# Kernel tuning notes

Measured on AMD Instinct MI355X. Metric: run time of the kernel, lower is better.

The kernel has to match this reference:

```python
import jax, jax.numpy as jnp
import numpy as np

B, S, HID, NH, DH = 2, 2048, 1024, 16, 64
NEG = jnp.float32(-1e-09)  # faithful to source: tiny negative, NOT -1e9


def _linear_params(key, fan_in, fan_out):
    k1, k2 = jax.random.split(key)
    lim = 1.0 / np.sqrt(fan_in)
    W = jax.random.uniform(k1, (fan_out, fan_in), jnp.float32, -lim, lim)
    b = jax.random.uniform(k2, (fan_out,), jnp.float32, -lim, lim)
    return W, b


def setup_inputs() -> dict:
    key = jax.random.key(0)
    ks = jax.random.split(key, 7)
    Q = jax.random.normal(ks[0], (B, S, HID), jnp.float32)
    K = jax.random.normal(ks[1], (B, S, HID), jnp.float32)
    V = jax.random.normal(ks[2], (B, S, HID), jnp.float32)
    pad_mask = jnp.ones((B, S), jnp.float32)
    attn_mask = jnp.tril(jnp.ones((S, S), jnp.float32))  # causal
    Wq, bq = _linear_params(ks[3], HID, HID)
    Wk, bk = _linear_params(ks[4], HID, HID)
    Wv, bv = _linear_params(ks[5], HID, HID)
    Wo, bo = _linear_params(ks[6], HID, HID)
    return {"Q": Q, "K": K, "V": V, "pad_mask": pad_mask, "attn_mask": attn_mask,
            "Wq": Wq, "bq": bq, "Wk": Wk, "bk": bk, "Wv": Wv, "bv": bv,
            "Wo": Wo, "bo": bo}


def reference(Q, K, V, pad_mask, attn_mask, Wq, bq, Wk, bk, Wv, bv, Wo, bo):
    def split_heads(x):  # [B,S,HID] -> [B,NH,S,DH]; matches torch.split+stack
        return x.reshape(B, S, NH, DH).transpose(0, 2, 1, 3)

    q = split_heads(Q @ Wq.T + bq)
    k = split_heads(K @ Wk.T + bk)
    v = split_heads(V @ Wv.T + bv)

    scores = jnp.einsum('bhqd,bhkd->bhqk', q, k) / np.sqrt(DH)
    # combined mask: pad outer-product * attn_mask (broadcast [S,S] -> [B,S,S])
    mask = pad_mask[:, :, None] * pad_mask[:, None, :] * attn_mask
    scores = jnp.where(mask[:, None, :, :] != 0, scores, NEG)
    attn = jax.nn.softmax(scores, axis=-1)

    ctx = jnp.einsum('bhqk,bhkd->bhqd', attn, v)
    ctx = ctx.transpose(0, 2, 1, 3).reshape(B, S, HID)  # concat heads
    return ctx @ Wo.T + bo
```

## Files before the change

### kernel.cpp

```cpp
#include <hip/hip_runtime.h>
#include <math.h>

#define BATCH 2
#define SLEN  2048
#define HIDD  1024
#define NHEAD 16
#define DHEAD 64
#define NEGV  (-1e-09f)

typedef __attribute__((ext_vector_type(8))) short bf16x8;
typedef __attribute__((ext_vector_type(4))) float f32x4;
typedef unsigned short u16;
typedef unsigned long long u64;

__device__ __forceinline__ u16 f2bf(float x) {
    unsigned u = __builtin_bit_cast(unsigned, x);
    return (u16)((u + 0x7fffu + ((u >> 16) & 1u)) >> 16);
}

#define GLD16(gp, lp) __builtin_amdgcn_global_load_lds(                      \
    (__attribute__((address_space(1))) void*)(gp),                           \
    (__attribute__((address_space(3))) void*)(lp), 16, 0, 0)

__global__ __launch_bounds__(256) void cvt_kernel(
    const float* __restrict__ s0, const float* __restrict__ s1,
    const float* __restrict__ s2, const float* __restrict__ s3,
    const float* __restrict__ s4, const float* __restrict__ s5,
    const float* __restrict__ s6,
    u16* __restrict__ d0, u16* __restrict__ d1, u16* __restrict__ d2,
    u16* __restrict__ d3, u16* __restrict__ d4, u16* __restrict__ d5,
    u16* __restrict__ d6)
{
    const float* sp; u16* dp; int n;
    switch (blockIdx.z) {
        case 0: sp = s0; dp = d0; n = 4194304; break;
        case 1: sp = s1; dp = d1; n = 4194304; break;
        case 2: sp = s2; dp = d2; n = 4194304; break;
        case 3: sp = s3; dp = d3; n = 1048576; break;
        case 4: sp = s4; dp = d4; n = 1048576; break;
        case 5: sp = s5; dp = d5; n = 1048576; break;
        default: sp = s6; dp = d6; n = 1048576; break;
    }
    const int idx = (blockIdx.x * 256 + threadIdx.x) * 8;
    if (idx >= n) return;
    const float4 a = *(const float4*)(sp + idx);
    const float4 c = *(const float4*)(sp + idx + 4);
    union { bf16x8 v; u16 u[8]; } o;
    o.u[0] = f2bf(a.x); o.u[1] = f2bf(a.y); o.u[2] = f2bf(a.z); o.u[3] = f2bf(a.w);
    o.u[4] = f2bf(c.x); o.u[5] = f2bf(c.y); o.u[6] = f2bf(c.z); o.u[7] = f2bf(c.w);
    *(bf16x8*)(dp + idx) = o.v;
}

template<int MODE>
__device__ __forceinline__ void gemm128(const u16* __restrict__ A,
                                        const u16* __restrict__ W,
                                        const float* __restrict__ bias,
                                        void* __restrict__ outp)
{
    __shared__ __align__(16) u16 sA[4096];
    __shared__ __align__(16) u16 sB[4096];
    const int t  = threadIdx.x;
    const int l  = t & 63, w = t >> 6;
    const int wr = w >> 1, wc = w & 1;
    const int m0 = blockIdx.y * 128, n0 = blockIdx.x * 128;

    f32x4 acc[4][4];
#pragma unroll
    for (int i = 0; i < 4; ++i)
#pragma unroll
        for (int j = 0; j < 4; ++j) acc[i][j] = (f32x4){0.f, 0.f, 0.f, 0.f};

    const int srow = t >> 2;
    const int scol = (t & 3) * 8;
    const u16* Ap = A + (size_t)(m0 + srow) * HIDD + scol;
    const u16* Wp = W + (size_t)(n0 + srow) * HIDD + scol;

    for (int k0 = 0; k0 < HIDD; k0 += 32) {
        __syncthreads();
        GLD16(Ap + k0,                      &sA[t * 8]);
        GLD16(Ap + k0 + (size_t)64 * HIDD,  &sA[2048 + t * 8]);
        GLD16(Wp + k0,                      &sB[t * 8]);
        GLD16(Wp + k0 + (size_t)64 * HIDD,  &sB[2048 + t * 8]);
        __syncthreads();

        bf16x8 af[4], bg[4];
#pragma unroll
        for (int i = 0; i < 4; ++i) {
            af[i] = *(const bf16x8*)&sA[(wr * 64 + i * 16 + (l & 15)) * 32 + (l >> 4) * 8];
            bg[i] = *(const bf16x8*)&sB[(wc * 64 + i * 16 + (l & 15)) * 32 + (l >> 4) * 8];
        }
#pragma unroll
        for (int mi = 0; mi < 4; ++mi)
#pragma unroll
            for (int ni = 0; ni < 4; ++ni)
                acc[mi][ni] = __builtin_amdgcn_mfma_f32_16x16x32_bf16(
                                  af[mi], bg[ni], acc[mi][ni], 0, 0, 0);
    }

    float bb[4];
#pragma unroll
    for (int ni = 0; ni < 4; ++ni) bb[ni] = bias[n0 + wc * 64 + ni * 16 + (l & 15)];

#pragma unroll
    for (int mi = 0; mi < 4; ++mi) {
#pragma unroll
        for (int ni = 0; ni < 4; ++ni) {
            const int n = n0 + wc * 64 + ni * 16 + (l & 15);
#pragma unroll
            for (int r = 0; r < 4; ++r) {
                const int m = m0 + wr * 64 + mi * 16 + (l >> 4) * 4 + r;
                const float v = acc[mi][ni][r] + bb[ni];
                if (MODE == 0) {
                    const int b = m >> 11, s = m & (SLEN - 1);
                    const int h = n >> 6,  d = n & (DHEAD - 1);
                    ((u16*)outp)[(((size_t)(b * NHEAD + h)) * SLEN + s) * DHEAD + d] = f2bf(v);
                } else {
                    ((float*)outp)[(size_t)m * HIDD + n] = v;
                }
            }
        }
    }
}

__global__ __launch_bounds__(256) void qkv_kernel(
    const u16* __restrict__ Qb, const u16* __restrict__ Kb, const u16* __restrict__ Vb,
    const u16* __restrict__ Wqb, const u16* __restrict__ Wkb, const u16* __restrict__ Wvb,
    const float* __restrict__ bq, const float* __restrict__ bk, const float* __restrict__ bv,
    u16* __restrict__ qh, u16* __restrict__ kh, u16* __restrict__ vh)
{
    if (blockIdx.z == 0)      gemm128<0>(Qb, Wqb, bq, qh);
    else if (blockIdx.z == 1) gemm128<0>(Kb, Wkb, bk, kh);
    else                      gemm128<0>(Vb, Wvb, bv, vh);
}

__global__ __launch_bounds__(256) void outproj_kernel(
    const u16* __restrict__ Cb, const u16* __restrict__ Wob,
    const float* __restrict__ bo, float* __restrict__ out)
{
    gemm128<1>(Cb, Wob, bo, out);
}

__global__ __launch_bounds__(256) void vtrans_kernel(const u16* __restrict__ vh,
                                                     u16* __restrict__ vt)
{
    const int bh = blockIdx.y, st = blockIdx.x, t = threadIdx.x;
    const u16* src = vh + ((size_t)bh * SLEN + st * 64) * DHEAD;
    u16* dst = vt + (size_t)bh * DHEAD * SLEN + st * 64;
    __shared__ u16 Ts[64][72];
#pragma unroll
    for (int it = 0; it < 2; ++it) {
        const int slot = t + it * 256;
        const int s = slot >> 3, c = (slot & 7) * 8;
        union { bf16x8 v; u16 u[8]; } x;
        x.v = *(const bf16x8*)(src + s * DHEAD + c);
#pragma unroll
        for (int j = 0; j < 8; ++j) Ts[c + j][s] = x.u[j];
    }
    __syncthreads();
#pragma unroll
    for (int it = 0; it < 2; ++it) {
        const int slot = t + it * 256;
        const int d = slot >> 3, c = (slot & 7) * 8;
        union { bf16x8 v; u16 u[8]; } x;
#pragma unroll
        for (int j = 0; j < 8; ++j) x.u[j] = Ts[d][c + j];
        *(bf16x8*)(dst + (size_t)d * SLEN + c) = x.v;
    }
}

__global__ __launch_bounds__(256) void mask_kernel(const float* __restrict__ pad,
                                                   const float* __restrict__ am,
                                                   u64* __restrict__ mb)
{
    const int gid = blockIdx.x * 256 + threadIdx.x;
    const int c = gid & 31;
    const int s = (gid >> 5) & (SLEN - 1);
    const int b = gid >> 16;
    const float padq = pad[b * SLEN + s];
    const float* amrow = am + (size_t)s * SLEN + c * 64;
    const float* pkp   = pad + b * SLEN + c * 64;
    u64 bits = 0;
#pragma unroll
    for (int j0 = 0; j0 < 64; j0 += 4) {
        const float4 a  = *(const float4*)(amrow + j0);
        const float4 pk = *(const float4*)(pkp + j0);
        if (padq * pk.x * a.x != 0.f) bits |= (1ull << (j0 + 0));
        if (padq * pk.y * a.y != 0.f) bits |= (1ull << (j0 + 1));
        if (padq * pk.z * a.z != 0.f) bits |= (1ull << (j0 + 2));
        if (padq * pk.w * a.w != 0.f) bits |= (1ull << (j0 + 3));
    }
    mb[((size_t)b * SLEN + s) * 32 + c] = bits;
}

__global__ __launch_bounds__(256) void flash_kernel(
    const u16* __restrict__ qh, const u16* __restrict__ kh,
    const u16* __restrict__ vt, const u64* __restrict__ mb,
    u16* __restrict__ cb)
{
    __shared__ __align__(16) char smem[24576];
    const int qt = blockIdx.x, h = blockIdx.y, b = blockIdx.z;
    const int t = threadIdx.x, l = t & 63, w = t >> 6;
    const int head = b * NHEAD + h;
    const u16* qp = qh + ((size_t)head * SLEN + qt * 64) * DHEAD;
    const u16* kp = kh + (size_t)head * SLEN * DHEAD;
    const u16* vp = vt + (size_t)head * DHEAD * SLEN;

    bf16x8 qf[2];
#pragma unroll
    for (int ks = 0; ks < 2; ++ks)
        qf[ks] = *(const bf16x8*)(qp + (w * 16 + (l & 15)) * DHEAD
                                     + ks * 32 + (l >> 4) * 8);

    f32x4 oacc[4];
    float mrun[4], lrun[4];
#pragma unroll
    for (int i = 0; i < 4; ++i) {
        oacc[i] = (f32x4){0.f, 0.f, 0.f, 0.f};
        mrun[i] = -INFINITY; lrun[i] = 0.f;
    }

    const int scb = (t & 7) * 16;

    for (int kt = 0; kt < SLEN / 64; ++kt) {
        bf16x8 kv[2], vv[2];
#pragma unroll
        for (int it = 0; it < 2; ++it) {
            const int row = (t >> 3) + it * 32;
            kv[it] = *(const bf16x8*)(kp + ((size_t)(kt * 64 + row)) * DHEAD + scb / 2);
            vv[it] = *(const bf16x8*)(vp + (size_t)row * SLEN + kt * 64 + scb / 2);
        }
        __syncthreads();
#pragma unroll
        for (int it = 0; it < 2; ++it) {
            const int row  = (t >> 3) + it * 32;
            const int byte = row * 128 + (scb ^ ((row & 7) << 4));
            *(bf16x8*)(smem + byte)        = kv[it];
            *(bf16x8*)(smem + 8192 + byte) = vv[it];
        }
        __syncthreads();

        f32x4 s4[4];
#pragma unroll
        for (int nf = 0; nf < 4; ++nf) s4[nf] = (f32x4){0.f, 0.f, 0.f, 0.f};
#pragma unroll
        for (int ks = 0; ks < 2; ++ks) {
#pragma unroll
            for (int nf = 0; nf < 4; ++nf) {
                const int kr = nf * 16 + (l & 15);
                const bf16x8 kf = *(const bf16x8*)(smem + kr * 128 +
                        ((ks * 64 + (l >> 4) * 16) ^ ((kr & 7) << 4)));
                s4[nf] = __builtin_amdgcn_mfma_f32_16x16x32_bf16(qf[ks], kf, s4[nf], 0, 0, 0);
            }
        }

        const int rbase = qt * 64 + w * 16 + (l >> 4) * 4;
        u64 bits[4];
#pragma unroll
        for (int r = 0; r < 4; ++r)
            bits[r] = mb[((size_t)b * SLEN + rbase + r) * 32 + kt];
#pragma unroll
        for (int r = 0; r < 4; ++r) {
            float sv[4];
#pragma unroll
            for (int nf = 0; nf < 4; ++nf) {
                const int bit = nf * 16 + (l & 15);
                sv[nf] = ((bits[r] >> bit) & 1ull) ? s4[nf][r] * 0.125f : NEGV;
            }
            float rm = fmaxf(fmaxf(sv[0], sv[1]), fmaxf(sv[2], sv[3]));
            rm = fmaxf(rm, __shfl_xor(rm, 1));
            rm = fmaxf(rm, __shfl_xor(rm, 2));
            rm = fmaxf(rm, __shfl_xor(rm, 4));
            rm = fmaxf(rm, __shfl_xor(rm, 8));
            const float mnew = fmaxf(mrun[r], rm);
            const float corr = __expf(mrun[r] - mnew);
            float p[4], rs = 0.f;
#pragma unroll
            for (int nf = 0; nf < 4; ++nf) { p[nf] = __expf(sv[nf] - mnew); rs += p[nf]; }
            rs += __shfl_xor(rs, 1);
            rs += __shfl_xor(rs, 2);
            rs += __shfl_xor(rs, 4);
            rs += __shfl_xor(rs, 8);
            lrun[r] = lrun[r] * corr + rs;
            mrun[r] = mnew;
#pragma unroll
            for (int nf = 0; nf < 4; ++nf) oacc[nf][r] *= corr;
            const int prow = (l >> 4) * 4 + r;
#pragma unroll
            for (int nf = 0; nf < 4; ++nf) {
                const int col = nf * 16 + (l & 15);
                *(u16*)(smem + 16384 + w * 2048 + prow * 128 +
                        ((col * 2) ^ ((prow & 7) << 4))) = f2bf(p[nf]);
            }
        }

#pragma unroll
        for (int ks = 0; ks < 2; ++ks) {
            const bf16x8 pf = *(const bf16x8*)(smem + 16384 + w * 2048 + (l & 15) * 128 +
                    ((ks * 64 + (l >> 4) * 16) ^ ((l & 7) << 4)));
#pragma unroll
            for (int nf = 0; nf < 4; ++nf) {
                const int vr = nf * 16 + (l & 15);
                const bf16x8 vf = *(const bf16x8*)(smem + 8192 + vr * 128 +
                        ((ks * 64 + (l >> 4) * 16) ^ ((vr & 7) << 4)));
                oacc[nf] = __builtin_amdgcn_mfma_f32_16x16x32_bf16(pf, vf, oacc[nf], 0, 0, 0);
            }
        }
        __syncthreads();
    }

#pragma unroll
    for (int r = 0; r < 4; ++r) {
        const float inv = 1.f / lrun[r];
        const int srow = qt * 64 + w * 16 + (l >> 4) * 4 + r;
#pragma unroll
        for (int nf = 0; nf < 4; ++nf) {
            const float v = oacc[nf][r] * inv;
            cb[((size_t)b * SLEN + srow) * HIDD + h * DHEAD + nf * 16 + (l & 15)] = f2bf(v);
        }
    }
}

extern "C" void kernel_launch(void* const* d_in, const int* in_sizes, int n_in,
                              void* d_out, int out_size, void* d_ws, size_t ws_size,
                              hipStream_t stream)
{
    (void)in_sizes; (void)n_in; (void)out_size; (void)ws_size;
    const float* Q   = (const float*)d_in[0];
    const float* K   = (const float*)d_in[1];
    const float* V   = (const float*)d_in[2];
    const float* pad = (const float*)d_in[3];
    const float* am  = (const float*)d_in[4];
    const float* Wq  = (const float*)d_in[5];
    const float* bq  = (const float*)d_in[6];
    const float* Wk  = (const float*)d_in[7];
    const float* bk  = (const float*)d_in[8];
    const float* Wv  = (const float*)d_in[9];
    const float* bv  = (const float*)d_in[10];
    const float* Wo  = (const float*)d_in[11];
    const float* bo  = (const float*)d_in[12];
    float* out = (float*)d_out;

    char* ws = (char*)d_ws;
    const size_t MB = 1u << 20;
    u16* Qb  = (u16*)(ws + 0);
    u16* Kb  = (u16*)(ws + 8  * MB);
    u16* Vb  = (u16*)(ws + 16 * MB);
    u16* Wqb = (u16*)(ws + 24 * MB);
    u16* Wkb = (u16*)(ws + 26 * MB);
    u16* Wvb = (u16*)(ws + 28 * MB);
    u16* Wob = (u16*)(ws + 30 * MB);
    u16* qhp = (u16*)(ws + 32 * MB);
    u16* khp = (u16*)(ws + 40 * MB);
    u16* vhp = (u16*)(ws + 48 * MB);
    u16* vtp = (u16*)(ws + 56 * MB);
    u64* mbp = (u64*)(ws + 64 * MB);
    u16* cbp = (u16*)(ws + 0);

    cvt_kernel<<<dim3(2048, 1, 7), 256, 0, stream>>>(Q, K, V, Wq, Wk, Wv, Wo,
                                                     Qb, Kb, Vb, Wqb, Wkb, Wvb, Wob);
    qkv_kernel<<<dim3(8, 32, 3), 256, 0, stream>>>(Qb, Kb, Vb, Wqb, Wkb, Wvb,
                                                   bq, bk, bv, qhp, khp, vhp);
    vtrans_kernel<<<dim3(32, 32), 256, 0, stream>>>(vhp, vtp);
    mask_kernel<<<dim3(512), 256, 0, stream>>>(pad, am, mbp);
    flash_kernel<<<dim3(32, 16, 2), 256, 0, stream>>>(qhp, khp, vtp, mbp, cbp);
    outproj_kernel<<<dim3(8, 32, 1), 256, 0, stream>>>(cbp, Wob, bo, out);
}
```

Measured before the change: 328.6 us.

## Compute transposed scores so each lane owns one query row for softmax

The QK^T MFMA now takes its operands in swapped order, producing S^T, so each lane holds all scores for a single query row. The online-softmax max and sum then need only two cross-lane shuffles per tile instead of four per row for four rows, and the mask needs one 64-bit load per lane instead of four. Per-row correction and normalisation factors are broadcast back to the output layout with __shfl. The trailing per-iteration __syncthreads is removed, relying on the barrier before the next shared-memory write to protect K/V reuse.

```diff
diff --git a/kernel.cpp b/kernel.cpp
--- a/kernel.cpp
+++ b/kernel.cpp
@@ -200,24 +200,22 @@
     __shared__ __align__(16) char smem[24576];
     const int qt = blockIdx.x, h = blockIdx.y, b = blockIdx.z;
     const int t = threadIdx.x, l = t & 63, w = t >> 6;
+    const int q = l & 15, hi = l >> 4;
     const int head = b * NHEAD + h;
     const u16* qp = qh + ((size_t)head * SLEN + qt * 64) * DHEAD;
     const u16* kp = kh + (size_t)head * SLEN * DHEAD;
     const u16* vp = vt + (size_t)head * DHEAD * SLEN;
+    const u64* mrow = mb + ((size_t)b * SLEN + qt * 64 + w * 16 + q) * 32;
 
     bf16x8 qf[2];
 #pragma unroll
     for (int ks = 0; ks < 2; ++ks)
-        qf[ks] = *(const bf16x8*)(qp + (w * 16 + (l & 15)) * DHEAD
-                                     + ks * 32 + (l >> 4) * 8);
+        qf[ks] = *(const bf16x8*)(qp + (w * 16 + q) * DHEAD + ks * 32 + hi * 8);
 
     f32x4 oacc[4];
-    float mrun[4], lrun[4];
-#pragma unroll
-    for (int i = 0; i < 4; ++i) {
-        oacc[i] = (f32x4){0.f, 0.f, 0.f, 0.f};
-        mrun[i] = -INFINITY; lrun[i] = 0.f;
-    }
+#pragma unroll
+    for (int i = 0; i < 4; ++i) oacc[i] = (f32x4){0.f, 0.f, 0.f, 0.f};
+    float mq = -INFINITY, lq = 0.f;
 
     const int scb = (t & 7) * 16;
 
@@ -239,83 +237,87 @@
         }
         __syncthreads();
 
-        f32x4 s4[4];
-#pragma unroll
-        for (int nf = 0; nf < 4; ++nf) s4[nf] = (f32x4){0.f, 0.f, 0.f, 0.f};
+        f32x4 s4t[4];
+#pragma unroll
+        for (int nf = 0; nf < 4; ++nf) s4t[nf] = (f32x4){0.f, 0.f, 0.f, 0.f};
 #pragma unroll
         for (int ks = 0; ks < 2; ++ks) {
 #pragma unroll
             for (int nf = 0; nf < 4; ++nf) {
-                const int kr = nf * 16 + (l & 15);
+                const int kr = nf * 16 + q;
                 const bf16x8 kf = *(const bf16x8*)(smem + kr * 128 +
-                        ((ks * 64 + (l >> 4) * 16) ^ ((kr & 7) << 4)));
-                s4[nf] = __builtin_amdgcn_mfma_f32_16x16x32_bf16(qf[ks], kf, s4[nf], 0, 0, 0);
-            }
-        }
-
-        const int rbase = qt * 64 + w * 16 + (l >> 4) * 4;
-        u64 bits[4];
-#pragma unroll
-        for (int r = 0; r < 4; ++r)
-            bits[r] = mb[((size_t)b * SLEN + rbase + r) * 32 + kt];
+                        ((ks * 64 + hi * 16) ^ ((kr & 7) << 4)));
+                s4t[nf] = __builtin_amdgcn_mfma_f32_16x16x32_bf16(kf, qf[ks], s4t[nf], 0, 0, 0);
+            }
+        }
+
+        const u64 bits = mrow[kt];
+        float p[4][4];
+        float rm = -INFINITY;
+#pragma unroll
+        for (int nf = 0; nf < 4; ++nf)
+#pragma unroll
+            for (int r = 0; r < 4; ++r) {
+                const int bit = nf * 16 + hi * 4 + r;
+                const float svv = ((bits >> bit) & 1ull) ? s4t[nf][r] * 0.125f : NEGV;
+                p[nf][r] = svv;
+                rm = fmaxf(rm, svv);
+            }
+        rm = fmaxf(rm, __shfl_xor(rm, 16));
+        rm = fmaxf(rm, __shfl_xor(rm, 32));
+        const float mnew = fmaxf(mq, rm);
+        const float corrq = __expf(mq - mnew);
+        float rs = 0.f;
+#pragma unroll
+        for (int nf = 0; nf < 4; ++nf)
+#pragma unroll
+            for (int r = 0; r < 4; ++r) {
+                p[nf][r] = __expf(p[nf][r] - mnew);
+                rs += p[nf][r];
+            }
+        rs += __shfl_xor(rs, 16);
+        rs += __shfl_xor(rs, 32);
+        lq = lq * corrq + rs;
+        mq = mnew;
+
+#pragma unroll
+        for (int nf = 0; nf < 4; ++nf)
+#pragma unroll
+            for (int r = 0; r < 4; ++r) {
+                const int kpos = nf * 16 + hi * 4 + r;
+                *(u16*)(smem + 16384 + w * 2048 + q * 128 +
+                        ((kpos * 2) ^ ((q & 7) << 4))) = f2bf(p[nf][r]);
+            }
+
 #pragma unroll
         for (int r = 0; r < 4; ++r) {
-            float sv[4];
+            const float cr = __shfl(corrq, hi * 4 + r);
+#pragma unroll
+            for (int nf = 0; nf < 4; ++nf) oacc[nf][r] *= cr;
+        }
+
+#pragma unroll
+        for (int ks = 0; ks < 2; ++ks) {
+            const bf16x8 pf = *(const bf16x8*)(smem + 16384 + w * 2048 + q * 128 +
+                    ((ks * 64 + hi * 16) ^ ((q & 7) << 4)));
 #pragma unroll
             for (int nf = 0; nf < 4; ++nf) {
-                const int bit = nf * 16 + (l & 15);
-                sv[nf] = ((bits[r] >> bit) & 1ull) ? s4[nf][r] * 0.125f : NEGV;
-            }
-            float rm = fmaxf(fmaxf(sv[0], sv[1]), fmaxf(sv[2], sv[3]));
-            rm = fmaxf(rm, __shfl_xor(rm, 1));
-            rm = fmaxf(rm, __shfl_xor(rm, 2));
-            rm = fmaxf(rm, __shfl_xor(rm, 4));
-            rm = fmaxf(rm, __shfl_xor(rm, 8));
-            const float mnew = fmaxf(mrun[r], rm);
-            const float corr = __expf(mrun[r] - mnew);
-            float p[4], rs = 0.f;
-#pragma unroll
-            for (int nf = 0; nf < 4; ++nf) { p[nf] = __expf(sv[nf] - mnew); rs += p[nf]; }
-            rs += __shfl_xor(rs, 1);
-            rs += __shfl_xor(rs, 2);
-            rs += __shfl_xor(rs, 4);
-            rs += __shfl_xor(rs, 8);
-            lrun[r] = lrun[r] * corr + rs;
-            mrun[r] = mnew;
-#pragma unroll
-            for (int nf = 0; nf < 4; ++nf) oacc[nf][r] *= corr;
-            const int prow = (l >> 4) * 4 + r;
-#pragma unroll
-            for (int nf = 0; nf < 4; ++nf) {
-                const int col = nf * 16 + (l & 15);
-                *(u16*)(smem + 16384 + w * 2048 + prow * 128 +
-                        ((col * 2) ^ ((prow & 7) << 4))) = f2bf(p[nf]);
-            }
-        }
-
-#pragma unroll
-        for (int ks = 0; ks < 2; ++ks) {
-            const bf16x8 pf = *(const bf16x8*)(smem + 16384 + w * 2048 + (l & 15) * 128 +
-                    ((ks * 64 + (l >> 4) * 16) ^ ((l & 7) << 4)));
-#pragma unroll
-            for (int nf = 0; nf < 4; ++nf) {
-                const int vr = nf * 16 + (l & 15);
+                const int vr = nf * 16 + q;
                 const bf16x8 vf = *(const bf16x8*)(smem + 8192 + vr * 128 +
-                        ((ks * 64 + (l >> 4) * 16) ^ ((vr & 7) << 4)));
+                        ((ks * 64 + hi * 16) ^ ((vr & 7) << 4)));
                 oacc[nf] = __builtin_amdgcn_mfma_f32_16x16x32_bf16(pf, vf, oacc[nf], 0, 0, 0);
             }
         }
-        __syncthreads();
     }
 
 #pragma unroll
     for (int r = 0; r < 4; ++r) {
-        const float inv = 1.f / lrun[r];
-        const int srow = qt * 64 + w * 16 + (l >> 4) * 4 + r;
+        const float linv = 1.f / __shfl(lq, hi * 4 + r);
+        const int srow = qt * 64 + w * 16 + hi * 4 + r;
 #pragma unroll
         for (int nf = 0; nf < 4; ++nf) {
-            const float v = oacc[nf][r] * inv;
-            cb[((size_t)b * SLEN + srow) * HIDD + h * DHEAD + nf * 16 + (l & 15)] = f2bf(v);
+            const float v = oacc[nf][r] * linv;
+            cb[((size_t)b * SLEN + srow) * HIDD + h * DHEAD + nf * 16 + q] = f2bf(v);
         }
     }
 }
```

Measured after the change: 313.3 us. 1.05x faster.
